# Kernel tuning notes

Hardware: AMD Instinct MI355X
Metric: run time of the kernel (lower is better)

The kernel has to match this reference:

```python
import jax, jax.numpy as jnp
import numpy as np
import math

D_MODEL = 1024
N_HEAD = 16
NUM_K = 170


def setup_inputs() -> dict:
    key = jax.random.key(0)
    ks = jax.random.split(key, 11)
    B, S, D = 2, 1024, D_MODEL
    scale = 1.0 / math.sqrt(D)
    inp = {
        "q": jax.random.normal(ks[0], (B, S, D), dtype=jnp.float32),
        "k": jax.random.normal(ks[1], (B, S, D), dtype=jnp.float32),
        "v": jax.random.normal(ks[2], (B, S, D), dtype=jnp.float32),
        # nn.Linear weights stored torch-style as (out, in); y = x @ W.T + b
        "wq": jax.random.normal(ks[3], (D, D), dtype=jnp.float32) * scale,
        "bq": jnp.zeros((D,), dtype=jnp.float32),
        "wk": jax.random.normal(ks[4], (D, D), dtype=jnp.float32) * scale,
        "bk": jnp.zeros((D,), dtype=jnp.float32),
        "wv": jax.random.normal(ks[5], (D, D), dtype=jnp.float32) * scale,
        "bv": jnp.zeros((D,), dtype=jnp.float32),
        "wo": jax.random.normal(ks[6], (D, D), dtype=jnp.float32) * scale,
        "bo": jnp.zeros((D,), dtype=jnp.float32),
    }
    return inp


def _split_heads(x):
    B, S, D = x.shape
    dh = D // N_HEAD
    return x.reshape(B, S, N_HEAD, dh).transpose(0, 2, 1, 3)  # [B,H,S,dh]


def reference(q, k, v, wq, bq, wk, bk, wv, bv, wo, bo):
    B, S, D = q.shape
    dh = D // N_HEAD
    qh = _split_heads(q @ wq.T + bq)
    kh = _split_heads(k @ wk.T + bk)
    vh = _split_heads(v @ wv.T + bv)
    # full QK^T scores [B,H,S,S]
    score = jnp.einsum("bhqd,bhkd->bhqk", qh, kh) / math.sqrt(dh)
    # topk threshold masking: keep only scores >= k-th largest per row
    num_k = min(NUM_K, S)
    topv = jax.lax.top_k(score, num_k)[0]           # [B,H,S,num_k], sorted desc
    thr = topv[..., -1:]                             # k-th largest value
    score = jnp.where(score < thr, jnp.float32(-1e18), score)
    attn = jax.nn.softmax(score, axis=-1)
    out = jnp.einsum("bhqk,bhkd->bhqd", attn, vh)   # [B,H,S,dh]
    out = out.transpose(0, 2, 1, 3).reshape(B, S, D)
    return out @ wo.T + bo
```

## Files before the change

### kernel.cpp

```cpp
#include <hip/hip_runtime.h>

typedef unsigned short u16;
typedef unsigned int   u32;
typedef short bf16x8 __attribute__((ext_vector_type(8)));
typedef float f32x4  __attribute__((ext_vector_type(4)));
typedef float f32x2  __attribute__((ext_vector_type(2)));

#define MFMA(a,b,c) __builtin_amdgcn_mfma_f32_16x16x32_bf16((a),(b),(c),0,0,0)
#define MB (1u<<20)

__device__ __forceinline__ u16 f2bf(float x) {
  u32 u = __builtin_bit_cast(u32, x);
  u32 r = (u + 0x7FFFu + ((u >> 16) & 1u)) >> 16;
  return (u16)r;
}
__device__ __forceinline__ float bf2f(u16 b) {
  u32 u = ((u32)b) << 16;
  return __builtin_bit_cast(float, u);
}
__device__ __forceinline__ void async16(void* lds, const void* g) {
  __builtin_amdgcn_global_load_lds(
      (const __attribute__((address_space(1))) u32*)g,
      (__attribute__((address_space(3))) u32*)lds, 16, 0, 0);
}


__global__ __launch_bounds__(256) void presplit_kernel(
    const float* q, const float* k, const float* v,
    const float* wq, const float* wk, const float* wv, const float* wo,
    char* ws)
{
  int y = blockIdx.y;
  const float* srcs[7] = {q, k, v, wq, wk, wv, wo};
  size_t hoffv = (y < 3) ? (size_t)y * (8*MB) : (size_t)(24*MB) + (size_t)(y-3) * (4*MB);
  size_t loffv = hoffv + ((y < 3) ? (size_t)(4*MB) : (size_t)(2*MB));
  bool wlo = (y == 0) || (y == 1) || (y == 3) || (y == 4);
  int n = (y < 3) ? (2*1024*1024) : (1024*1024);
  int idx = (blockIdx.x * 256 + threadIdx.x) * 4;
  if (idx >= n) return;
  float4 x = *(const float4*)(srcs[y] + idx);
  ushort4 hv; hv.x = f2bf(x.x); hv.y = f2bf(x.y); hv.z = f2bf(x.z); hv.w = f2bf(x.w);
  *(ushort4*)(ws + hoffv + (size_t)idx * 2) = hv;
  if (wlo) {
    ushort4 lv;
    lv.x = f2bf(x.x - bf2f(hv.x)); lv.y = f2bf(x.y - bf2f(hv.y));
    lv.z = f2bf(x.z - bf2f(hv.z)); lv.w = f2bf(x.w - bf2f(hv.w));
    *(ushort4*)(ws + loffv + (size_t)idx * 2) = lv;
  }
}

#define PA_H 0
#define PA_L 16384
#define PB_H 32768
#define PB_L 49152
#define PROJ_LDS 65536

__global__ __launch_bounds__(512, 4) void proj_kernel(char* ws,
    const float* bq, const float* bk, const float* bv)
{
  __shared__ __align__(16) char smem[PROJ_LDS];
  const int bid = blockIdx.x;
  const int z = (bid < 256) ? (bid & 1) : 2;
  const int tile = (bid < 256) ? (bid >> 1) : (bid - 256);
  const bool split = (z < 2);
  const u16* Ah = (const u16*)(ws + (size_t)z*(8*MB));
  const u16* Al = (const u16*)(ws + (size_t)z*(8*MB) + 4*MB);
  const u16* Bh = (const u16*)(ws + (size_t)(24*MB) + (size_t)z*(4*MB));
  const u16* Bl = (const u16*)(ws + (size_t)(24*MB) + (size_t)z*(4*MB) + 2*MB);
  u16* Oh = (u16*)(ws + (size_t)(40*MB) + (size_t)z*(8*MB));
  u16* Ol = (u16*)(ws + (size_t)(40*MB) + (size_t)z*(8*MB) + 4*MB);
  const float* bias = (z == 0) ? bq : ((z == 1) ? bk : bv);
  const float scale = (z == 0) ? 0.125f : 1.0f;

  const int t = threadIdx.x, w = t >> 6, lane = t & 63;
  const int l15 = lane & 15, l4 = lane >> 4;
  const int m0 = (tile >> 3) * 128;
  const int n0 = (tile & 7) * 128;
  const int mw = (w >> 2) * 64, nw = (w & 3) * 32;

  f32x4 acc[4][2];
  const f32x4 z4 = {0.f, 0.f, 0.f, 0.f};
  #pragma unroll
  for (int i = 0; i < 4; ++i)
    #pragma unroll
    for (int j = 0; j < 2; ++j) acc[i][j] = z4;

  for (int kt = 0; kt < 16; ++kt) {
    __syncthreads();
    #pragma unroll
    for (int i = 0; i < 2; ++i) {
      int chunk = w*128 + i*64 + lane;
      int row = chunk >> 3, seg = chunk & 7;
      int ss = seg ^ (row & 7);
      size_t ga = (size_t)(m0 + row) * 1024 + kt*64 + ss*8;
      size_t gb = (size_t)(n0 + row) * 1024 + kt*64 + ss*8;
      async16(smem + PA_H + chunk*16, Ah + ga);
      async16(smem + PB_H + chunk*16, Bh + gb);
      if (split) {
        async16(smem + PA_L + chunk*16, Al + ga);
        async16(smem + PB_L + chunk*16, Bl + gb);
      }
    }
    __syncthreads();
    #pragma unroll
    for (int kf = 0; kf < 2; ++kf) {
      bf16x8 avh[4], avl[4], bvh[2], bvl[2];
      #pragma unroll
      for (int mf = 0; mf < 4; ++mf) {
        int row = mw + mf*16 + l15;
        int ks = kf*4 + l4;
        int off = row*128 + ((ks ^ (row & 7)) << 4);
        avh[mf] = *(const bf16x8*)(smem + PA_H + off);
        if (split) avl[mf] = *(const bf16x8*)(smem + PA_L + off);
      }
      #pragma unroll
      for (int nf = 0; nf < 2; ++nf) {
        int row = nw + nf*16 + l15;
        int ks = kf*4 + l4;
        int off = row*128 + ((ks ^ (row & 7)) << 4);
        bvh[nf] = *(const bf16x8*)(smem + PB_H + off);
        if (split) bvl[nf] = *(const bf16x8*)(smem + PB_L + off);
      }
      #pragma unroll
      for (int mf = 0; mf < 4; ++mf)
        #pragma unroll
        for (int nf = 0; nf < 2; ++nf) {
          acc[mf][nf] = MFMA(avh[mf], bvh[nf], acc[mf][nf]);
          if (split) {
            acc[mf][nf] = MFMA(avh[mf], bvl[nf], acc[mf][nf]);
            acc[mf][nf] = MFMA(avl[mf], bvh[nf], acc[mf][nf]);
          }
        }
    }
  }
  #pragma unroll
  for (int mf = 0; mf < 4; ++mf)
    #pragma unroll
    for (int nf = 0; nf < 2; ++nf) {
      int colg = n0 + nw + nf*16 + l15;
      float bb = bias[colg];
      #pragma unroll
      for (int r = 0; r < 4; ++r) {
        int rowg = m0 + mw + mf*16 + l4*4 + r;
        float val = (acc[mf][nf][r] + bb) * scale;
        u16 hb = f2bf(val);
        if (z == 2) {
          Oh[(size_t)rowg * 1024 + colg] = hb;
        } else {
          int bq_ = rowg >> 10, s = rowg & 1023;
          int hh = colg >> 6, d = colg & 63;
          int bh2 = bq_*16 + hh;
          int reg = d >> 5, l4s = (d & 31) >> 3, de = d & 7;
          int lane2 = l4s*16 + (s & 15);
          size_t o;
          if (z == 0) o = ((size_t)((bh2*64 + (s >> 4))*2 + reg))*512 + lane2*8 + de;
          else        o = ((size_t)(((bh2*8 + (s >> 7))*8 + ((s >> 4) & 7))*2 + reg))*512 + lane2*8 + de;
          Oh[o] = hb;
          Ol[o] = f2bf(val - bf2f(hb));
        }
      }
    }
}

#define FB_OFF 8192
#define FIN_LDS 16384

__global__ __launch_bounds__(256, 2) void final_kernel(char* ws, const float* bo, float* out)
{
  __shared__ __align__(16) char smem[FIN_LDS];
  const u16* Ah = (const u16*)(ws + (size_t)(8*MB));
  const u16* Bh = (const u16*)(ws + (size_t)(36*MB));
  const int t = threadIdx.x, w = t >> 6, lane = t & 63;
  const int l15 = lane & 15, l4 = lane >> 4;
  const int m0 = (blockIdx.x >> 4) * 64;
  const int n0 = (blockIdx.x & 15) * 64;
  const int mw = (w >> 1) * 32, nw = (w & 1) * 32;

  f32x4 acc[2][2];
  const f32x4 z4 = {0.f, 0.f, 0.f, 0.f};
  #pragma unroll
  for (int i = 0; i < 2; ++i)
    #pragma unroll
    for (int j = 0; j < 2; ++j) acc[i][j] = z4;

  for (int kt = 0; kt < 16; ++kt) {
    __syncthreads();
    #pragma unroll
    for (int i = 0; i < 2; ++i) {
      int chunk = t + i*256;
      int row = chunk >> 3, seg = chunk & 7;
      int ss = seg ^ (row & 7);
      async16(smem + chunk*16, Ah + (size_t)(m0 + row) * 1024 + kt*64 + ss*8);
      async16(smem + FB_OFF + chunk*16, Bh + (size_t)(n0 + row) * 1024 + kt*64 + ss*8);
    }
    __syncthreads();
    #pragma unroll
    for (int kf = 0; kf < 2; ++kf) {
      bf16x8 avh[2], bvh[2];
      #pragma unroll
      for (int mf = 0; mf < 2; ++mf) {
        int row = mw + mf*16 + l15;
        int ks = kf*4 + l4;
        avh[mf] = *(const bf16x8*)(smem + row*128 + ((ks ^ (row & 7)) << 4));
      }
      #pragma unroll
      for (int nf = 0; nf < 2; ++nf) {
        int row = nw + nf*16 + l15;
        int ks = kf*4 + l4;
        bvh[nf] = *(const bf16x8*)(smem + FB_OFF + row*128 + ((ks ^ (row & 7)) << 4));
      }
      #pragma unroll
      for (int mf = 0; mf < 2; ++mf)
        #pragma unroll
        for (int nf = 0; nf < 2; ++nf)
          acc[mf][nf] = MFMA(avh[mf], bvh[nf], acc[mf][nf]);
    }
  }
  #pragma unroll
  for (int mf = 0; mf < 2; ++mf)
    #pragma unroll
    for (int nf = 0; nf < 2; ++nf) {
      int colg = n0 + nw + nf*16 + l15;
      float bb = bo[colg];
      #pragma unroll
      for (int r = 0; r < 4; ++r) {
        int rowg = m0 + mw + mf*16 + l4*4 + r;
        out[(size_t)rowg * 1024 + colg] = acc[mf][nf][r] + bb;
      }
    }
}

__global__ __launch_bounds__(256) void vtrans_kernel(char* ws)
{
  __shared__ u16 th[64][68];
  const u16* Vph = (const u16*)(ws + (size_t)(56*MB));
  u16* Vf = (u16*)(ws + 0);
  int id = blockIdx.x;
  int bh = id >> 4, sc = id & 15;
  int b = bh >> 4, h = bh & 15;
  int t = threadIdx.x;
  #pragma unroll
  for (int j = 0; j < 16; ++j) {
    int e = t + 256*j;
    int sr = e >> 6, dc = e & 63;
    th[sr][dc] = Vph[(size_t)(b*1024 + sc*64 + sr) * 1024 + h*64 + dc];
  }
  __syncthreads();
  #pragma unroll
  for (int j = 0; j < 16; ++j) {
    int e = t + 256*j;
    int dr = e >> 6, scl = e & 63;
    int s = sc*64 + scl;
    int f = dr >> 4, l15v = dr & 15;
    int half = s >> 9, ks = (s >> 5) & 15, l4v = (s >> 3) & 3, de = s & 7;
    size_t o = ((size_t)(((bh*4 + f)*2 + half)*16 + ks))*512 + (l4v*16 + l15v)*8 + de;
    Vf[o] = th[scl][dr];
  }
}

#define CB_STRIDE 528
#define CB_SZ     8448
#define P_STRIDE  2064
#define PART_OFF  33024
#define ATT_LDS   (PART_OFF + 4096)
#define KSEL 170

__global__ __launch_bounds__(512, 6) void attn_kernel(char* ws)
{
  __shared__ __align__(16) char smem[ATT_LDS];
  const u16* Qh  = (const u16*)(ws + (size_t)(40*MB));
  const u16* Ql  = (const u16*)(ws + (size_t)(44*MB));
  const u16* Kh  = (const u16*)(ws + (size_t)(48*MB));
  const u16* Kl  = (const u16*)(ws + (size_t)(52*MB));
  const u16* Vf  = (const u16*)(ws + 0);
  u16* Ath = (u16*)(ws + (size_t)(8*MB));

  int t = threadIdx.x, w = t >> 6, lane = t & 63;
  int l15 = lane & 15, l4 = lane >> 4;
  int bid = blockIdx.x;
  int logical = (bid & 7) * 256 + (bid >> 3);
  int bh = logical >> 6, qt = logical & 63;
  int b = bh >> 4, h = bh & 15;
  int q0 = qt * 16;

  const f32x4 z4 = {0.f, 0.f, 0.f, 0.f};

  bf16x8 kf[4];
#define LOADKC(KC) do { \
    size_t kb2 = ((size_t)(((bh*8 + (KC))*8 + w)*2))*512 + lane*8; \
    kf[0] = *(const bf16x8*)(Kh + kb2); \
    kf[1] = *(const bf16x8*)(Kh + kb2 + 512); \
    kf[2] = *(const bf16x8*)(Kl + kb2); \
    kf[3] = *(const bf16x8*)(Kl + kb2 + 512); \
  } while (0)

  LOADKC(0);

  bf16x8 qfh[2], qfl[2];
  {
    size_t qb2 = ((size_t)((bh*64 + qt)*2))*512 + lane*8;
    qfh[0] = *(const bf16x8*)(Qh + qb2);
    qfh[1] = *(const bf16x8*)(Qh + qb2 + 512);
    qfl[0] = *(const bf16x8*)(Ql + qb2);
    qfl[1] = *(const bf16x8*)(Ql + qb2 + 512);
  }

  f32x2 va[8], vb[8];
  #pragma unroll
  for (int kc = 0; kc < 8; ++kc) {
    f32x4 a0 = z4, a1 = z4;
    a0 = MFMA(qfh[0], kf[0], a0);
    a1 = MFMA(qfh[1], kf[1], a1);
    a0 = MFMA(qfl[0], kf[0], a0);
    a1 = MFMA(qfl[1], kf[1], a1);
    a0 = MFMA(qfh[0], kf[2], a0);
    a1 = MFMA(qfh[1], kf[3], a1);
    if (kc < 7) LOADKC(kc + 1);
    #pragma unroll
    for (int r_ = 0; r_ < 4; ++r_)
      *(float*)(smem + (kc & 1)*CB_SZ + (l4*4 + r_)*CB_STRIDE + (w*16 + l15)*4)
          = a0[r_] + a1[r_];
    asm volatile("s_waitcnt lgkmcnt(0)" ::: "memory");
    __builtin_amdgcn_s_barrier();
    asm volatile("" ::: "memory");
    va[kc] = *(const f32x2*)(smem + (kc & 1)*CB_SZ + w*CB_STRIDE + lane*8);
    vb[kc] = *(const f32x2*)(smem + (kc & 1)*CB_SZ + (w + 8)*CB_STRIDE + lane*8);
  }
  __syncthreads();

  int f = w & 3, half = w >> 2;
  size_t vbase = ((size_t)(((bh*4 + f)*2 + half)*16))*512 + lane*8;
  bf16x8 vv[2][4];
#define LOADV(BUF, G) do { \
    _Pragma("unroll") \
    for (int j_ = 0; j_ < 4; ++j_) \
      vv[BUF][j_] = *(const bf16x8*)(Vf + vbase + (size_t)((G)*4 + j_)*512); \
    } while (0)

  {
    float mA = va[0][0], mB = vb[0][0];
    #pragma unroll
    for (int i = 0; i < 8; ++i)
      #pragma unroll
      for (int e = 0; e < 2; ++e) {
        mA = fmaxf(mA, va[i][e]);
        mB = fmaxf(mB, vb[i][e]);
      }
    #pragma unroll
    for (int off = 32; off > 0; off >>= 1) {
      mA = fmaxf(mA, __shfl_xor(mA, off));
      mB = fmaxf(mB, __shfl_xor(mB, off));
    }

    float loA = mA - 16.f, hiA = mA, cLoA = 1024.f, cHiA = 1.f;
    float loB = mB - 16.f, hiB = mB, cLoB = 1024.f, cHiB = 1.f;
    float thrA = 0.f, thrB = 0.f;
    bool fA = false, fB = false;
    #pragma unroll 1
    for (int it = 0; it < 32 && !(fA && fB); ++it) {
      float gA, gB;
      if (it < 8) {
        gA = fminf(fmaxf((cLoA - (float)KSEL) / fmaxf(cLoA - cHiA, 1.f), 0.10f), 0.90f);
        gB = fminf(fmaxf((cLoB - (float)KSEL) / fmaxf(cLoB - cHiB, 1.f), 0.10f), 0.90f);
      } else {
        gA = 0.5f; gB = 0.5f;
      }
      float tA = loA + (hiA - loA) * gA;
      float tB = loB + (hiB - loB) * gB;
      if (!(tA > loA && tA < hiA)) { if (!fA) { thrA = loA; fA = true; } tA = loA; }
      if (!(tB > loB && tB < hiB)) { if (!fB) { thrB = loB; fB = true; } tB = loB; }
      int cA = 0, cB = 0;
      #pragma unroll
      for (int i = 0; i < 8; ++i)
        #pragma unroll
        for (int e = 0; e < 2; ++e) {
          cA += (int)__popcll(__ballot(va[i][e] >= tA));
          cB += (int)__popcll(__ballot(vb[i][e] >= tB));
        }
      if (!fA) {
        if (cA == KSEL) { thrA = tA; fA = true; }
        else if (cA > KSEL) { loA = tA; cLoA = (float)cA; }
        else { hiA = tA; cHiA = (float)cA; }
      }
      if (!fB) {
        if (cB == KSEL) { thrB = tB; fB = true; }
        else if (cB > KSEL) { loB = tB; cLoB = (float)cB; }
        else { hiB = tB; cHiB = (float)cB; }
      }
    }
    if (!fA) thrA = loA;
    if (!fB) thrB = loB;

    LOADV(0, 0);

    float sA = 0.f, sB = 0.f;
    #pragma unroll
    for (int i = 0; i < 8; ++i)
      #pragma unroll
      for (int e = 0; e < 2; ++e) {
        float xa = va[i][e], xb = vb[i][e];
        float ea = (xa >= thrA) ? __expf(xa - mA) : 0.f;
        float eb = (xb >= thrB) ? __expf(xb - mB) : 0.f;
        va[i][e] = ea; vb[i][e] = eb;
        sA += ea; sB += eb;
      }
    #pragma unroll
    for (int off = 32; off > 0; off >>= 1) {
      sA += __shfl_xor(sA, off);
      sB += __shfl_xor(sB, off);
    }
    float rA_ = 1.f / sA, rB_ = 1.f / sB;

    #pragma unroll
    for (int i = 0; i < 8; ++i) {
      u32 pwA = (u32)f2bf(va[i][0] * rA_) | ((u32)f2bf(va[i][1] * rA_) << 16);
      u32 pwB = (u32)f2bf(vb[i][0] * rB_) | ((u32)f2bf(vb[i][1] * rB_) << 16);
      *(u32*)(smem + w*P_STRIDE       + i*256 + lane*4) = pwA;
      *(u32*)(smem + (w + 8)*P_STRIDE + i*256 + lane*4) = pwB;
    }
  }
  __syncthreads();

  LOADV(1, 1);
  f32x4 ac0 = z4, ac1 = z4;
  #pragma unroll
  for (int g = 0; g < 4; ++g) {
    #pragma unroll
    for (int j = 0; j < 4; ++j) {
      int ksl = g*4 + j;
      bf16x8 pa = *(const bf16x8*)(smem + l15*P_STRIDE + (half*16 + ksl)*64 + l4*16);
      if (j & 1) ac1 = MFMA(pa, vv[g & 1][j], ac1);
      else       ac0 = MFMA(pa, vv[g & 1][j], ac0);
    }
    if (g == 0) LOADV(0, 2);
    if (g == 1) LOADV(1, 3);
  }
  f32x4 a = ac0 + ac1;

  if (half == 1)
    *(f32x4*)(smem + PART_OFF + (f*64 + lane)*16) = a;
  __syncthreads();
  if (half == 0) {
    f32x4 o4 = *(const f32x4*)(smem + PART_OFF + (f*64 + lane)*16);
    #pragma unroll
    for (int r = 0; r < 4; ++r) {
      float val = a[r] + o4[r];
      size_t o = (size_t)(b*1024 + q0 + l4*4 + r) * 1024 + h*64 + f*16 + l15;
      Ath[o] = f2bf(val);
    }
  }
}

extern "C" void kernel_launch(void* const* d_in, const int* in_sizes, int n_in,
                              void* d_out, int out_size, void* d_ws, size_t ws_size,
                              hipStream_t stream)
{
  const float* q  = (const float*)d_in[0];
  const float* k  = (const float*)d_in[1];
  const float* v  = (const float*)d_in[2];
  const float* wq = (const float*)d_in[3];
  const float* bq = (const float*)d_in[4];
  const float* wk = (const float*)d_in[5];
  const float* bk = (const float*)d_in[6];
  const float* wv = (const float*)d_in[7];
  const float* bv = (const float*)d_in[8];
  const float* wo = (const float*)d_in[9];
  const float* bo = (const float*)d_in[10];
  float* out = (float*)d_out;
  char* ws = (char*)d_ws;
  if (ws_size < (64ull << 20)) return;

  presplit_kernel<<<dim3(2048, 7), 256, 0, stream>>>(q, k, v, wq, wk, wv, wo, ws);
  proj_kernel<<<384, 512, 0, stream>>>(ws, bq, bk, bv);
  vtrans_kernel<<<512, 256, 0, stream>>>(ws);
  attn_kernel<<<2048, 512, 0, stream>>>(ws);
  final_kernel<<<512, 256, 0, stream>>>(ws, bo, out);
}
```

Before: 133.4 us.

## Fuse V transpose into projection epilogue and skip counting for converged rows

The V projection epilogue now writes its output directly in the fragment-transposed layout the attention kernel consumes. This removes the separate vtrans kernel launch and its extra pass through global memory. The top-k threshold search now evaluates each row's ballot count only while that row is unconverged, so a finished row stops paying for counting. In exchange the V projection does scattered 2-byte stores instead of row-contiguous ones.

```diff
diff --git a/kernel.cpp b/kernel.cpp
--- a/kernel.cpp
+++ b/kernel.cpp
@@ -144,12 +144,16 @@
         int rowg = m0 + mw + mf*16 + l4*4 + r;
         float val = (acc[mf][nf][r] + bb) * scale;
         u16 hb = f2bf(val);
+        int bq_ = rowg >> 10, s = rowg & 1023;
+        int hh = colg >> 6, d = colg & 63;
+        int bh2 = bq_*16 + hh;
         if (z == 2) {
-          Oh[(size_t)rowg * 1024 + colg] = hb;
+          int fb = d >> 4, l15v = d & 15;
+          int half = s >> 9, ks = (s >> 5) & 15, l4v = (s >> 3) & 3, de = s & 7;
+          size_t o = ((size_t)(((bh2*4 + fb)*2 + half)*16 + ks))*512
+                     + (l4v*16 + l15v)*8 + de;
+          Oh[o] = hb;
         } else {
-          int bq_ = rowg >> 10, s = rowg & 1023;
-          int hh = colg >> 6, d = colg & 63;
-          int bh2 = bq_*16 + hh;
           int reg = d >> 5, l4s = (d & 31) >> 3, de = d & 7;
           int lane2 = l4s*16 + (s & 15);
           size_t o;
@@ -230,34 +234,6 @@
     }
 }
 
-__global__ __launch_bounds__(256) void vtrans_kernel(char* ws)
-{
-  __shared__ u16 th[64][68];
-  const u16* Vph = (const u16*)(ws + (size_t)(56*MB));
-  u16* Vf = (u16*)(ws + 0);
-  int id = blockIdx.x;
-  int bh = id >> 4, sc = id & 15;
-  int b = bh >> 4, h = bh & 15;
-  int t = threadIdx.x;
-  #pragma unroll
-  for (int j = 0; j < 16; ++j) {
-    int e = t + 256*j;
-    int sr = e >> 6, dc = e & 63;
-    th[sr][dc] = Vph[(size_t)(b*1024 + sc*64 + sr) * 1024 + h*64 + dc];
-  }
-  __syncthreads();
-  #pragma unroll
-  for (int j = 0; j < 16; ++j) {
-    int e = t + 256*j;
-    int dr = e >> 6, scl = e & 63;
-    int s = sc*64 + scl;
-    int f = dr >> 4, l15v = dr & 15;
-    int half = s >> 9, ks = (s >> 5) & 15, l4v = (s >> 3) & 3, de = s & 7;
-    size_t o = ((size_t)(((bh*4 + f)*2 + half)*16 + ks))*512 + (l4v*16 + l15v)*8 + de;
-    Vf[o] = th[scl][dr];
-  }
-}
-
 #define CB_STRIDE 528
 #define CB_SZ     8448
 #define P_STRIDE  2064
@@ -272,7 +248,7 @@
   const u16* Ql  = (const u16*)(ws + (size_t)(44*MB));
   const u16* Kh  = (const u16*)(ws + (size_t)(48*MB));
   const u16* Kl  = (const u16*)(ws + (size_t)(52*MB));
-  const u16* Vf  = (const u16*)(ws + 0);
+  const u16* Vf  = (const u16*)(ws + (size_t)(56*MB));
   u16* Ath = (u16*)(ws + (size_t)(8*MB));
 
   int t = threadIdx.x, w = t >> 6, lane = t & 63;
@@ -358,34 +334,41 @@
     bool fA = false, fB = false;
     #pragma unroll 1
     for (int it = 0; it < 32 && !(fA && fB); ++it) {
-      float gA, gB;
-      if (it < 8) {
-        gA = fminf(fmaxf((cLoA - (float)KSEL) / fmaxf(cLoA - cHiA, 1.f), 0.10f), 0.90f);
-        gB = fminf(fmaxf((cLoB - (float)KSEL) / fmaxf(cLoB - cHiB, 1.f), 0.10f), 0.90f);
-      } else {
-        gA = 0.5f; gB = 0.5f;
-      }
-      float tA = loA + (hiA - loA) * gA;
-      float tB = loB + (hiB - loB) * gB;
-      if (!(tA > loA && tA < hiA)) { if (!fA) { thrA = loA; fA = true; } tA = loA; }
-      if (!(tB > loB && tB < hiB)) { if (!fB) { thrB = loB; fB = true; } tB = loB; }
-      int cA = 0, cB = 0;
-      #pragma unroll
-      for (int i = 0; i < 8; ++i)
-        #pragma unroll
-        for (int e = 0; e < 2; ++e) {
-          cA += (int)__popcll(__ballot(va[i][e] >= tA));
-          cB += (int)__popcll(__ballot(vb[i][e] >= tB));
+      if (!fA) {
+        float gA = (it < 8)
+          ? fminf(fmaxf((cLoA - (float)KSEL) / fmaxf(cLoA - cHiA, 1.f), 0.10f), 0.90f)
+          : 0.5f;
+        float tA = loA + (hiA - loA) * gA;
+        if (!(tA > loA && tA < hiA)) { thrA = loA; fA = true; }
+        else {
+          int cA = 0;
+          #pragma unroll
+          for (int i = 0; i < 8; ++i)
+            #pragma unroll
+            for (int e = 0; e < 2; ++e)
+              cA += (int)__popcll(__ballot(va[i][e] >= tA));
+          if (cA == KSEL) { thrA = tA; fA = true; }
+          else if (cA > KSEL) { loA = tA; cLoA = (float)cA; }
+          else { hiA = tA; cHiA = (float)cA; }
         }
-      if (!fA) {
-        if (cA == KSEL) { thrA = tA; fA = true; }
-        else if (cA > KSEL) { loA = tA; cLoA = (float)cA; }
-        else { hiA = tA; cHiA = (float)cA; }
       }
       if (!fB) {
-        if (cB == KSEL) { thrB = tB; fB = true; }
-        else if (cB > KSEL) { loB = tB; cLoB = (float)cB; }
-        else { hiB = tB; cHiB = (float)cB; }
+        float gB = (it < 8)
+          ? fminf(fmaxf((cLoB - (float)KSEL) / fmaxf(cLoB - cHiB, 1.f), 0.10f), 0.90f)
+          : 0.5f;
+        float tB = loB + (hiB - loB) * gB;
+        if (!(tB > loB && tB < hiB)) { thrB = loB; fB = true; }
+        else {
+          int cB = 0;
+          #pragma unroll
+          for (int i = 0; i < 8; ++i)
+            #pragma unroll
+            for (int e = 0; e < 2; ++e)
+              cB += (int)__popcll(__ballot(vb[i][e] >= tB));
+          if (cB == KSEL) { thrB = tB; fB = true; }
+          else if (cB > KSEL) { loB = tB; cLoB = (float)cB; }
+          else { hiB = tB; cHiB = (float)cB; }
+        }
       }
     }
     if (!fA) thrA = loA;
@@ -472,7 +455,6 @@
 
   presplit_kernel<<<dim3(2048, 7), 256, 0, stream>>>(q, k, v, wq, wk, wv, wo, ws);
   proj_kernel<<<384, 512, 0, stream>>>(ws, bq, bk, bv);
-  vtrans_kernel<<<512, 256, 0, stream>>>(ws);
   attn_kernel<<<2048, 512, 0, stream>>>(ws);
   final_kernel<<<512, 256, 0, stream>>>(ws, bo, out);
 }
```

Result: no change. 133.0 us (-0.3%).
